# Optimization experiments

Hardware: AMD Instinct MI355X
Metric: run time of the kernel (lower is better)

## Reference

```python
import jax, jax.numpy as jnp
import numpy as np

# fastmax config (scalar flags fused into the original CUDA kernel)
MASK = True          # causal masking
DROPOUT = 0.1        # dropout noise scale
NORMALIZE = True     # l2-normalize q and k
TEMPERATURE = 1.0    # score temperature


def setup_inputs() -> dict:
    key = jax.random.key(0)
    ks = jax.random.split(key, 5)
    b, h, n, d = 4, 16, 1024, 64
    q = jax.random.normal(ks[0], (b, h, n, d), jnp.float32)
    k = jax.random.normal(ks[1], (b, h, n, d), jnp.float32)
    v = jax.random.normal(ks[2], (b, h, n, d), jnp.float32)
    drop_noise = jax.random.normal(ks[3], (b, h, n, d), jnp.float32)
    rpe_matrix = jax.random.normal(ks[4], (2 * n - 1, d), jnp.float32)
    return {"q": q, "k": k, "v": v, "drop_noise": drop_noise, "rpe_matrix": rpe_matrix}


def _fastmax(q, k, v, drop_noise, rpe_matrix):
    # fastmax: first-order Taylor linearization of softmax attention,
    # a_ij = (1 + q_i.k_j/t + q_i.rpe[i-j+n-1]/t) / sum_j(...), with causal
    # masking done by zeroing scores (not -inf) and dropout noise fused in.
    b, h, n, d = q.shape
    if NORMALIZE:
        q = q / jnp.linalg.norm(q, axis=-1, keepdims=True)
        k = k / jnp.linalg.norm(k, axis=-1, keepdims=True)
    # dropout noise fused into values
    v = v + DROPOUT * drop_noise
    # base Taylor scores: 1 + qk/t  -> [b,h,n,n]
    scores = 1.0 + jnp.einsum('bhid,bhjd->bhij', q, k) / TEMPERATURE
    # relative positional encoding bias: q_i . rpe[i-j+n-1]
    qr = jnp.einsum('bhid,rd->bhir', q, rpe_matrix)           # [b,h,n,2n-1]
    idx = jnp.arange(n)
    rel = idx[:, None] - idx[None, :] + (n - 1)               # [n,n] in [0, 2n-2]
    bias = jnp.take_along_axis(qr, jnp.broadcast_to(rel, (b, h, n, n)), axis=-1)
    scores = scores + bias / TEMPERATURE
    if MASK:
        causal = (idx[:, None] >= idx[None, :]).astype(scores.dtype)  # [n,n]
        scores = scores * causal
    denom = jnp.sum(scores, axis=-1, keepdims=True)           # [b,h,n,1]
    out = jnp.einsum('bhij,bhjd->bhid', scores, v) / denom
    return out


def reference(q, k, v, drop_noise, rpe_matrix):
    return _fastmax(q, k, v, drop_noise, rpe_matrix)
```

## Files before the change

### kernel.cpp

```cpp
#include <hip/hip_runtime.h>


constexpr int N   = 1024;
constexpr int D   = 64;
constexpr int NBH = 64;
constexpr int LDT = 72;

constexpr size_t KH_OFF = 0;
constexpr size_t KL_OFF = KH_OFF + (size_t)NBH * N * D * 2;
constexpr size_t VH_OFF = KL_OFF + (size_t)NBH * N * D * 2;
constexpr size_t VL_OFF = VH_OFF + (size_t)NBH * N * D * 2;
constexpr size_t RH_OFF = VL_OFF + (size_t)NBH * N * D * 2;
constexpr size_t RL_OFF = RH_OFF + (size_t)2048 * D * 2;

typedef short short8  __attribute__((ext_vector_type(8)));
typedef float float4v __attribute__((ext_vector_type(4)));

#define LDS_FENCE() asm volatile("s_waitcnt lgkmcnt(0)" ::: "memory")

__device__ __forceinline__ ushort f2bf(float x) {
    union { float f; unsigned u; } un; un.f = x;
    unsigned r = un.u + 0x7fffu + ((un.u >> 16) & 1u);
    return (ushort)(r >> 16);
}
__device__ __forceinline__ float bf2f(ushort h) {
    union { unsigned u; float f; } un; un.u = ((unsigned)h) << 16;
    return un.f;
}
__device__ __forceinline__ void split2(float x, ushort& h, ushort& l) {
    h = f2bf(x);
    l = f2bf(x - bf2f(h));
}
__device__ __forceinline__ void pack16(const float* v, ushort* dh, ushort* dl) {
    ushort hh[16], ll[16];
#pragma unroll
    for (int j = 0; j < 16; ++j) split2(v[j], hh[j], ll[j]);
    uint4 a, b;
    a.x = hh[0] | (hh[1] << 16);  a.y = hh[2] | (hh[3] << 16);
    a.z = hh[4] | (hh[5] << 16);  a.w = hh[6] | (hh[7] << 16);
    b.x = hh[8] | (hh[9] << 16);  b.y = hh[10] | (hh[11] << 16);
    b.z = hh[12] | (hh[13] << 16); b.w = hh[14] | (hh[15] << 16);
    ((uint4*)dh)[0] = a; ((uint4*)dh)[1] = b;
    a.x = ll[0] | (ll[1] << 16);  a.y = ll[2] | (ll[3] << 16);
    a.z = ll[4] | (ll[5] << 16);  a.w = ll[6] | (ll[7] << 16);
    b.x = ll[8] | (ll[9] << 16);  b.y = ll[10] | (ll[11] << 16);
    b.z = ll[12] | (ll[13] << 16); b.w = ll[14] | (ll[15] << 16);
    ((uint4*)dl)[0] = a; ((uint4*)dl)[1] = b;
}

__global__ __launch_bounds__(256) void prep_k(const float* __restrict__ kg,
                                              ushort* __restrict__ kh,
                                              ushort* __restrict__ kl) {
    const int bh = blockIdx.y;
    const int row = blockIdx.x * 64 + (threadIdx.x >> 2);
    const int seg = threadIdx.x & 3;
    const float4* p = (const float4*)(kg + ((size_t)bh * N + row) * D + seg * 16);
    float4 f[4] = {p[0], p[1], p[2], p[3]};
    float ss = 0.f;
#pragma unroll
    for (int i = 0; i < 4; ++i)
        ss += f[i].x * f[i].x + f[i].y * f[i].y + f[i].z * f[i].z + f[i].w * f[i].w;
    ss += __shfl_xor(ss, 1, 4);
    ss += __shfl_xor(ss, 2, 4);
    const float rn = rsqrtf(ss);
    float v[16];
#pragma unroll
    for (int i = 0; i < 4; ++i) {
        v[4 * i + 0] = f[i].x * rn; v[4 * i + 1] = f[i].y * rn;
        v[4 * i + 2] = f[i].z * rn; v[4 * i + 3] = f[i].w * rn;
    }
    const size_t o = ((size_t)bh * N + row) * D + seg * 16;
    pack16(v, kh + o, kl + o);
}

__global__ __launch_bounds__(256) void prep_rpe(const float* __restrict__ rg,
                                                ushort* __restrict__ rh,
                                                ushort* __restrict__ rl) {
    const int row = blockIdx.x * 64 + (threadIdx.x >> 2);
    if (row >= 2 * N - 1) return;
    const int seg = threadIdx.x & 3;
    const float4* p = (const float4*)(rg + (size_t)row * D + seg * 16);
    float4 f[4] = {p[0], p[1], p[2], p[3]};
    float v[16];
#pragma unroll
    for (int i = 0; i < 4; ++i) {
        v[4 * i + 0] = f[i].x; v[4 * i + 1] = f[i].y;
        v[4 * i + 2] = f[i].z; v[4 * i + 3] = f[i].w;
    }
    const size_t o = (size_t)row * D + seg * 16;
    pack16(v, rh + o, rl + o);
}

__global__ __launch_bounds__(256) void prep_v(const float* __restrict__ vg,
                                              const float* __restrict__ ng,
                                              ushort* __restrict__ vh,
                                              ushort* __restrict__ vl) {
    __shared__ ushort Th[64 * 72], Tl[64 * 72];
    const int bh = blockIdx.y, c0 = blockIdx.x * 64;
    const int cl = threadIdx.x >> 2, seg = threadIdx.x & 3;
    {
        const float4* pv = (const float4*)(vg + ((size_t)bh * N + c0 + cl) * D + seg * 16);
        const float4* pn = (const float4*)(ng + ((size_t)bh * N + c0 + cl) * D + seg * 16);
#pragma unroll
        for (int i = 0; i < 4; ++i) {
            float4 fv = pv[i], fn = pn[i];
            float va[4] = {fv.x + 0.1f * fn.x, fv.y + 0.1f * fn.y,
                           fv.z + 0.1f * fn.z, fv.w + 0.1f * fn.w};
#pragma unroll
            for (int j = 0; j < 4; ++j) {
                ushort hh, ll;
                split2(va[j], hh, ll);
                const int dc = seg * 16 + i * 4 + j;
                Th[dc * 72 + cl] = hh;
                Tl[dc * 72 + cl] = ll;
            }
        }
    }
    __syncthreads();
    {
        const int dc = threadIdx.x >> 2;
        const size_t o = ((size_t)bh * D + dc) * N + c0 + seg * 16;
        uint4* sh = (uint4*)&Th[dc * 72 + seg * 16];
        uint4* sl = (uint4*)&Tl[dc * 72 + seg * 16];
        ((uint4*)(vh + o))[0] = sh[0]; ((uint4*)(vh + o))[1] = sh[1];
        ((uint4*)(vl + o))[0] = sl[0]; ((uint4*)(vl + o))[1] = sl[1];
    }
}

__device__ __forceinline__ float4v mfma6(short8 ah0, short8 ah1, short8 al0, short8 al1,
                                         const ushort* ph, const ushort* pl, float4v c) {
    short8 bh0 = *(const short8*)ph;
    short8 bh1 = *(const short8*)(ph + 32);
    short8 bl0 = *(const short8*)pl;
    short8 bl1 = *(const short8*)(pl + 32);
    c = __builtin_amdgcn_mfma_f32_16x16x32_bf16(ah0, bh0, c, 0, 0, 0);
    c = __builtin_amdgcn_mfma_f32_16x16x32_bf16(ah1, bh1, c, 0, 0, 0);
    c = __builtin_amdgcn_mfma_f32_16x16x32_bf16(ah0, bl0, c, 0, 0, 0);
    c = __builtin_amdgcn_mfma_f32_16x16x32_bf16(ah1, bl1, c, 0, 0, 0);
    c = __builtin_amdgcn_mfma_f32_16x16x32_bf16(al0, bh0, c, 0, 0, 0);
    c = __builtin_amdgcn_mfma_f32_16x16x32_bf16(al1, bh1, c, 0, 0, 0);
    return c;
}

__global__ __launch_bounds__(256, 4)
void fastmax_main(const float* __restrict__ qg,
                  const ushort* __restrict__ kh, const ushort* __restrict__ kl,
                  const ushort* __restrict__ vh, const ushort* __restrict__ vl,
                  const ushort* __restrict__ rh, const ushort* __restrict__ rl,
                  float* __restrict__ og) {
    __shared__ __align__(16) char smem[73728];
    ushort* Kh = (ushort*)smem;
    ushort* Kl = Kh + 64 * LDT;
    ushort* Rh = Kl + 64 * LDT;
    ushort* Rl = Rh + 128 * LDT;
    ushort* Vh = Rl + 128 * LDT;
    ushort* Vl = Vh + 64 * LDT;

    const int tid  = threadIdx.x;
    const int lane = tid & 63;
    const int wv   = tid >> 6;
    const int bh   = blockIdx.y;
    const int x    = lane & 15;
    const int quad = lane >> 4;
    const int band = wv * 16;

    float*  Bst = (float*)(smem + wv * 5760);
    ushort* Sh  = (ushort*)(smem + wv * 5760);
    ushort* Sl  = Sh + 16 * LDT;

    const ushort* khb = kh + (size_t)bh * N * D;
    const ushort* klb = kl + (size_t)bh * N * D;
    const ushort* vhb = vh + (size_t)bh * D * N;
    const ushort* vlb = vl + (size_t)bh * D * N;

    for (int half = 0; half < 2; ++half) {
        const int bix = half == 0 ? (int)blockIdx.x + 8 : 7 - (int)blockIdx.x;
        const int i0  = bix * 64;

        const float* qrow = qg + ((size_t)bh * N + i0 + band + x) * D;
        float qf[16];
        *(float4*)&qf[0]  = *(const float4*)(qrow + quad * 8);
        *(float4*)&qf[4]  = *(const float4*)(qrow + quad * 8 + 4);
        *(float4*)&qf[8]  = *(const float4*)(qrow + 32 + quad * 8);
        *(float4*)&qf[12] = *(const float4*)(qrow + 32 + quad * 8 + 4);
        float ss = 0.f;
#pragma unroll
        for (int j = 0; j < 16; ++j) ss += qf[j] * qf[j];
        ss += __shfl_xor(ss, 16);
        ss += __shfl_xor(ss, 32);
        const float rn = rsqrtf(ss);
        short8 qh0, ql0, qh1, ql1;
#pragma unroll
        for (int j = 0; j < 8; ++j) {
            ushort h, l;
            split2(qf[j] * rn, h, l);      qh0[j] = (short)h; ql0[j] = (short)l;
            split2(qf[8 + j] * rn, h, l);  qh1[j] = (short)h; ql1[j] = (short)l;
        }

        float4v oacc[4];
#pragma unroll
        for (int i = 0; i < 4; ++i) oacc[i] = (float4v){0.f, 0.f, 0.f, 0.f};
        float pden[4] = {0.f, 0.f, 0.f, 0.f};

        for (int jt = 0; jt <= bix; ++jt) {
            const int j0   = jt * 64;
            const int rel0 = i0 - j0 + N - 64;

            {
                const ushort* gKh = khb + (size_t)j0 * D;
                const ushort* gKl = klb + (size_t)j0 * D;
                const ushort* gVh = vhb + j0;
                const ushort* gVl = vlb + j0;
                for (int u = tid; u < 512; u += 256) {
                    const int row = u >> 3, c8 = (u & 7) * 8;
                    *(uint4*)&Kh[row * LDT + c8] = *(const uint4*)&gKh[row * D + c8];
                    *(uint4*)&Kl[row * LDT + c8] = *(const uint4*)&gKl[row * D + c8];
                    *(uint4*)&Vh[row * LDT + c8] = *(const uint4*)&gVh[(size_t)row * N + c8];
                    *(uint4*)&Vl[row * LDT + c8] = *(const uint4*)&gVl[(size_t)row * N + c8];
                }
                const ushort* gRh = rh + (size_t)rel0 * D;
                const ushort* gRl = rl + (size_t)rel0 * D;
                for (int u = tid; u < 1024; u += 256) {
                    const int row = u >> 3, c8 = (u & 7) * 8;
                    *(uint4*)&Rh[row * LDT + c8] = *(const uint4*)&gRh[row * D + c8];
                    *(uint4*)&Rl[row * LDT + c8] = *(const uint4*)&gRl[row * D + c8];
                }
            }
            __syncthreads();

            float4v sacc[4];
#pragma unroll
            for (int nt = 0; nt < 4; ++nt) {
                const int off = (nt * 16 + x) * LDT + quad * 8;
                float4v c = (float4v){0.f, 0.f, 0.f, 0.f};
                sacc[nt] = mfma6(qh0, qh1, ql0, ql1, &Kh[off], &Kl[off], c);
            }
            float4v racc[5];
#pragma unroll
            for (int t = 0; t < 5; ++t) {
                const int off = (band + t * 16 + x) * LDT + quad * 8;
                float4v c = (float4v){0.f, 0.f, 0.f, 0.f};
                racc[t] = mfma6(qh0, qh1, ql0, ql1, &Rh[off], &Rl[off], c);
            }
            __syncthreads();

#pragma unroll
            for (int t = 0; t < 5; ++t) {
                float* p = &Bst[(t * 16 + x) * 18 + quad * 4];
                float2 a; a.x = racc[t][0]; a.y = racc[t][1];
                float2 b; b.x = racc[t][2]; b.y = racc[t][3];
                *(float2*)p = a;
                *(float2*)(p + 2) = b;
            }
            LDS_FENCE();

            const bool diag = (jt == bix);
            float s[4][4];
#pragma unroll
            for (int nt = 0; nt < 4; ++nt) {
#pragma unroll
                for (int rr = 0; rr < 4; ++rr) {
                    const int rt = band + quad * 4 + rr;
                    const int ct = nt * 16 + x;
                    const int wl = rt - ct + 63 - band;
                    float val = sacc[nt][rr] + Bst[wl * 18 + quad * 4 + rr] + 1.0f;
                    if (diag && ct > rt) val = 0.f;
                    pden[rr] += val;
                    s[nt][rr] = val;
                }
            }
            LDS_FENCE();

#pragma unroll
            for (int nt = 0; nt < 4; ++nt)
#pragma unroll
                for (int rr = 0; rr < 4; ++rr) {
                    ushort hh, ll;
                    split2(s[nt][rr], hh, ll);
                    Sh[(quad * 4 + rr) * LDT + nt * 16 + x] = hh;
                    Sl[(quad * 4 + rr) * LDT + nt * 16 + x] = ll;
                }
            LDS_FENCE();
            const short8 sh0 = *(const short8*)&Sh[x * LDT + quad * 8];
            const short8 sh1 = *(const short8*)&Sh[x * LDT + 32 + quad * 8];
            const short8 sl0 = *(const short8*)&Sl[x * LDT + quad * 8];
            const short8 sl1 = *(const short8*)&Sl[x * LDT + 32 + quad * 8];

#pragma unroll
            for (int nt = 0; nt < 4; ++nt) {
                const int off = (nt * 16 + x) * LDT + quad * 8;
                oacc[nt] = mfma6(sh0, sh1, sl0, sl1, &Vh[off], &Vl[off], oacc[nt]);
            }
            __syncthreads();
        }

        float inv[4];
#pragma unroll
        for (int rr = 0; rr < 4; ++rr) {
            float d = pden[rr];
            d += __shfl_xor(d, 1, 16);
            d += __shfl_xor(d, 2, 16);
            d += __shfl_xor(d, 4, 16);
            d += __shfl_xor(d, 8, 16);
            inv[rr] = 1.0f / d;
        }
        float* outp = og + ((size_t)bh * N + i0 + band) * D;
#pragma unroll
        for (int nt = 0; nt < 4; ++nt)
#pragma unroll
            for (int rr = 0; rr < 4; ++rr)
                outp[(size_t)(quad * 4 + rr) * D + nt * 16 + x] = oacc[nt][rr] * inv[rr];
    }
}

extern "C" void kernel_launch(void* const* d_in, const int* in_sizes, int n_in,
                              void* d_out, int out_size, void* d_ws, size_t ws_size,
                              hipStream_t stream) {
    const float* q   = (const float*)d_in[0];
    const float* k   = (const float*)d_in[1];
    const float* v   = (const float*)d_in[2];
    const float* dn  = (const float*)d_in[3];
    const float* rpe = (const float*)d_in[4];
    float* out = (float*)d_out;
    char* ws = (char*)d_ws;

    ushort* kh = (ushort*)(ws + KH_OFF);
    ushort* kl = (ushort*)(ws + KL_OFF);
    ushort* vh = (ushort*)(ws + VH_OFF);
    ushort* vl = (ushort*)(ws + VL_OFF);
    ushort* rh = (ushort*)(ws + RH_OFF);
    ushort* rl = (ushort*)(ws + RL_OFF);

    prep_k  <<<dim3(N / 64, NBH), 256, 0, stream>>>(k, kh, kl);
    prep_v  <<<dim3(N / 64, NBH), 256, 0, stream>>>(v, dn, vh, vl);
    prep_rpe<<<dim3(32), 256, 0, stream>>>(rpe, rh, rl);
    fastmax_main<<<dim3(8, NBH), 256, 0, stream>>>(q, kh, kl, vh, vl, rh, rl, out);
}
```

Baseline: 196.7 us.

## Fuse K/V/RPE preprocessing into main attention kernel as single launch

Removes the three separate prep kernels (K normalization and bf16 hi/lo split, V plus dropout-noise transpose and split, RPE split). Each block of one flattened 512-block launch now prepares, for its own head, only the K/V tiles and RPE rows its causal range needs, writing them to the workspace before running the attention loop. This is meant to cut launch overhead and the separate prep passes. In exchange, the prep work is repeated by every block sharing a head and by all blocks for RPE, which multiplies global traffic. Several blocks also write identical workspace data concurrently, and the RPE loop for the last pair reads one row past the 2n-1 valid rows.

Result: slower. 227.8 us (+15.8%).

```diff
diff --git a/kernel.cpp b/kernel.cpp
--- a/kernel.cpp
+++ b/kernel.cpp
@@ -46,85 +46,6 @@
     b.x = ll[8] | (ll[9] << 16);  b.y = ll[10] | (ll[11] << 16);
     b.z = ll[12] | (ll[13] << 16); b.w = ll[14] | (ll[15] << 16);
     ((uint4*)dl)[0] = a; ((uint4*)dl)[1] = b;
-}
-
-__global__ __launch_bounds__(256) void prep_k(const float* __restrict__ kg,
-                                              ushort* __restrict__ kh,
-                                              ushort* __restrict__ kl) {
-    const int bh = blockIdx.y;
-    const int row = blockIdx.x * 64 + (threadIdx.x >> 2);
-    const int seg = threadIdx.x & 3;
-    const float4* p = (const float4*)(kg + ((size_t)bh * N + row) * D + seg * 16);
-    float4 f[4] = {p[0], p[1], p[2], p[3]};
-    float ss = 0.f;
-#pragma unroll
-    for (int i = 0; i < 4; ++i)
-        ss += f[i].x * f[i].x + f[i].y * f[i].y + f[i].z * f[i].z + f[i].w * f[i].w;
-    ss += __shfl_xor(ss, 1, 4);
-    ss += __shfl_xor(ss, 2, 4);
-    const float rn = rsqrtf(ss);
-    float v[16];
-#pragma unroll
-    for (int i = 0; i < 4; ++i) {
-        v[4 * i + 0] = f[i].x * rn; v[4 * i + 1] = f[i].y * rn;
-        v[4 * i + 2] = f[i].z * rn; v[4 * i + 3] = f[i].w * rn;
-    }
-    const size_t o = ((size_t)bh * N + row) * D + seg * 16;
-    pack16(v, kh + o, kl + o);
-}
-
-__global__ __launch_bounds__(256) void prep_rpe(const float* __restrict__ rg,
-                                                ushort* __restrict__ rh,
-                                                ushort* __restrict__ rl) {
-    const int row = blockIdx.x * 64 + (threadIdx.x >> 2);
-    if (row >= 2 * N - 1) return;
-    const int seg = threadIdx.x & 3;
-    const float4* p = (const float4*)(rg + (size_t)row * D + seg * 16);
-    float4 f[4] = {p[0], p[1], p[2], p[3]};
-    float v[16];
-#pragma unroll
-    for (int i = 0; i < 4; ++i) {
-        v[4 * i + 0] = f[i].x; v[4 * i + 1] = f[i].y;
-        v[4 * i + 2] = f[i].z; v[4 * i + 3] = f[i].w;
-    }
-    const size_t o = (size_t)row * D + seg * 16;
-    pack16(v, rh + o, rl + o);
-}
-
-__global__ __launch_bounds__(256) void prep_v(const float* __restrict__ vg,
-                                              const float* __restrict__ ng,
-                                              ushort* __restrict__ vh,
-                                              ushort* __restrict__ vl) {
-    __shared__ ushort Th[64 * 72], Tl[64 * 72];
-    const int bh = blockIdx.y, c0 = blockIdx.x * 64;
-    const int cl = threadIdx.x >> 2, seg = threadIdx.x & 3;
-    {
-        const float4* pv = (const float4*)(vg + ((size_t)bh * N + c0 + cl) * D + seg * 16);
-        const float4* pn = (const float4*)(ng + ((size_t)bh * N + c0 + cl) * D + seg * 16);
-#pragma unroll
-        for (int i = 0; i < 4; ++i) {
-            float4 fv = pv[i], fn = pn[i];
-            float va[4] = {fv.x + 0.1f * fn.x, fv.y + 0.1f * fn.y,
-                           fv.z + 0.1f * fn.z, fv.w + 0.1f * fn.w};
-#pragma unroll
-            for (int j = 0; j < 4; ++j) {
-                ushort hh, ll;
-                split2(va[j], hh, ll);
-                const int dc = seg * 16 + i * 4 + j;
-                Th[dc * 72 + cl] = hh;
-                Tl[dc * 72 + cl] = ll;
-            }
-        }
-    }
-    __syncthreads();
-    {
-        const int dc = threadIdx.x >> 2;
-        const size_t o = ((size_t)bh * D + dc) * N + c0 + seg * 16;
-        uint4* sh = (uint4*)&Th[dc * 72 + seg * 16];
-        uint4* sl = (uint4*)&Tl[dc * 72 + seg * 16];
-        ((uint4*)(vh + o))[0] = sh[0]; ((uint4*)(vh + o))[1] = sh[1];
-        ((uint4*)(vl + o))[0] = sl[0]; ((uint4*)(vl + o))[1] = sl[1];
-    }
 }
 
 __device__ __forceinline__ float4v mfma6(short8 ah0, short8 ah1, short8 al0, short8 al1,
@@ -143,12 +64,98 @@
 }
 
 __global__ __launch_bounds__(256, 4)
-void fastmax_main(const float* __restrict__ qg,
-                  const ushort* __restrict__ kh, const ushort* __restrict__ kl,
-                  const ushort* __restrict__ vh, const ushort* __restrict__ vl,
-                  const ushort* __restrict__ rh, const ushort* __restrict__ rl,
-                  float* __restrict__ og) {
+void fastmax_one(const float* __restrict__ qg, const float* __restrict__ kg,
+                 const float* __restrict__ vg, const float* __restrict__ ng,
+                 const float* __restrict__ rg,
+                 ushort* __restrict__ kh, ushort* __restrict__ kl,
+                 ushort* __restrict__ vh, ushort* __restrict__ vl,
+                 ushort* __restrict__ rh, ushort* __restrict__ rl,
+                 float* __restrict__ og) {
     __shared__ __align__(16) char smem[73728];
+    const int tid  = threadIdx.x;
+    const int flat = blockIdx.x;
+    const int pair = flat >> 6;
+    const int bh   = flat & 63;
+    const int nTiles = pair + 9;
+
+    ushort* khb = kh + (size_t)bh * N * D;
+    ushort* klb = kl + (size_t)bh * N * D;
+    ushort* vhb = vh + (size_t)bh * D * N;
+    ushort* vlb = vl + (size_t)bh * D * N;
+
+    {
+        const float* kgb = kg + (size_t)bh * N * D;
+        for (int u = tid; u < nTiles * 256; u += 256) {
+            const int gr = u >> 2, seg = u & 3;
+            const float4* p = (const float4*)(kgb + (size_t)gr * D + seg * 16);
+            float4 f[4] = {p[0], p[1], p[2], p[3]};
+            float ss = 0.f;
+#pragma unroll
+            for (int i = 0; i < 4; ++i)
+                ss += f[i].x * f[i].x + f[i].y * f[i].y + f[i].z * f[i].z + f[i].w * f[i].w;
+            ss += __shfl_xor(ss, 1, 4);
+            ss += __shfl_xor(ss, 2, 4);
+            const float rn = rsqrtf(ss);
+            float v[16];
+#pragma unroll
+            for (int i = 0; i < 4; ++i) {
+                v[4 * i + 0] = f[i].x * rn; v[4 * i + 1] = f[i].y * rn;
+                v[4 * i + 2] = f[i].z * rn; v[4 * i + 3] = f[i].w * rn;
+            }
+            const size_t o = (size_t)gr * D + seg * 16;
+            pack16(v, khb + o, klb + o);
+        }
+        const int rTasks = (pair + 10) * 64 * 4;
+        for (int u = tid; u < rTasks; u += 256) {
+            const int row = 960 + (u >> 2), seg = u & 3;
+            const float4* p = (const float4*)(rg + (size_t)row * D + seg * 16);
+            float4 f[4] = {p[0], p[1], p[2], p[3]};
+            float v[16];
+#pragma unroll
+            for (int i = 0; i < 4; ++i) {
+                v[4 * i + 0] = f[i].x; v[4 * i + 1] = f[i].y;
+                v[4 * i + 2] = f[i].z; v[4 * i + 3] = f[i].w;
+            }
+            const size_t o = (size_t)row * D + seg * 16;
+            pack16(v, rh + o, rl + o);
+        }
+        ushort* Th = (ushort*)smem;
+        ushort* Tl = Th + 64 * 72;
+        for (int tv = 0; tv < nTiles; ++tv) {
+            const int c0 = tv * 64;
+            const int cl = tid >> 2, seg = tid & 3;
+            {
+                const float4* pv = (const float4*)(vg + ((size_t)bh * N + c0 + cl) * D + seg * 16);
+                const float4* pn = (const float4*)(ng + ((size_t)bh * N + c0 + cl) * D + seg * 16);
+#pragma unroll
+                for (int i = 0; i < 4; ++i) {
+                    float4 fv = pv[i], fn = pn[i];
+                    float va[4] = {fv.x + 0.1f * fn.x, fv.y + 0.1f * fn.y,
+                                   fv.z + 0.1f * fn.z, fv.w + 0.1f * fn.w};
+#pragma unroll
+                    for (int j = 0; j < 4; ++j) {
+                        ushort hh, ll;
+                        split2(va[j], hh, ll);
+                        const int dc = seg * 16 + i * 4 + j;
+                        Th[dc * 72 + cl] = hh;
+                        Tl[dc * 72 + cl] = ll;
+                    }
+                }
+            }
+            __syncthreads();
+            {
+                const int dc = tid >> 2;
+                const size_t o = (size_t)dc * N + c0 + seg * 16;
+                uint4* sh = (uint4*)&Th[dc * 72 + seg * 16];
+                uint4* sl = (uint4*)&Tl[dc * 72 + seg * 16];
+                ((uint4*)(vhb + o))[0] = sh[0]; ((uint4*)(vhb + o))[1] = sh[1];
+                ((uint4*)(vlb + o))[0] = sl[0]; ((uint4*)(vlb + o))[1] = sl[1];
+            }
+            __syncthreads();
+        }
+    }
+    __syncthreads();
+
     ushort* Kh = (ushort*)smem;
     ushort* Kl = Kh + 64 * LDT;
     ushort* Rh = Kl + 64 * LDT;
@@ -156,10 +163,8 @@
     ushort* Vh = Rl + 128 * LDT;
     ushort* Vl = Vh + 64 * LDT;
 
-    const int tid  = threadIdx.x;
     const int lane = tid & 63;
     const int wv   = tid >> 6;
-    const int bh   = blockIdx.y;
     const int x    = lane & 15;
     const int quad = lane >> 4;
     const int band = wv * 16;
@@ -168,13 +173,8 @@
     ushort* Sh  = (ushort*)(smem + wv * 5760);
     ushort* Sl  = Sh + 16 * LDT;
 
-    const ushort* khb = kh + (size_t)bh * N * D;
-    const ushort* klb = kl + (size_t)bh * N * D;
-    const ushort* vhb = vh + (size_t)bh * D * N;
-    const ushort* vlb = vl + (size_t)bh * D * N;
-
     for (int half = 0; half < 2; ++half) {
-        const int bix = half == 0 ? (int)blockIdx.x + 8 : 7 - (int)blockIdx.x;
+        const int bix = half == 0 ? pair + 8 : 7 - pair;
         const int i0  = bix * 64;
 
         const float* qrow = qg + ((size_t)bh * N + i0 + band + x) * D;
@@ -331,8 +331,6 @@
     ushort* rh = (ushort*)(ws + RH_OFF);
     ushort* rl = (ushort*)(ws + RL_OFF);
 
-    prep_k  <<<dim3(N / 64, NBH), 256, 0, stream>>>(k, kh, kl);
-    prep_v  <<<dim3(N / 64, NBH), 256, 0, stream>>>(v, dn, vh, vl);
-    prep_rpe<<<dim3(32), 256, 0, stream>>>(rpe, rh, rl);
-    fastmax_main<<<dim3(8, NBH), 256, 0, stream>>>(q, kh, kl, vh, vl, rh, rl, out);
-}
+    fastmax_one<<<dim3(512), dim3(256), 0, stream>>>(q, k, v, dn, rpe,
+                                                     kh, kl, vh, vl, rh, rl, out);
+}
```
